# Optimization experiments

Hardware: AMD Instinct MI355X
Metric: run time of the kernel (lower is better)

## Reference

```python
import jax, jax.numpy as jnp
import numpy as np

N = 50000       # nodes
E = 800000      # edges
IN = 64         # input node feature dim
H = 4           # attention heads
C = 32          # per-head channels (h_dim)
HC = H * C      # 128, concat output per conv
ED = 16         # edge feature dim
G = 2000        # number of graphs (molecules)
NEG = 0.2       # GATConv negative slope


def setup_inputs() -> dict:
    key = jax.random.key(0)
    ks = jax.random.split(key, 40)
    rn = lambda k, shp, s=0.1: (jax.random.normal(k, shp, jnp.float32) * s)
    inp = {}
    inp["x"] = jax.random.normal(ks[0], (N, IN), jnp.float32)
    inp["edge_index"] = jax.random.randint(ks[1], (2, E), 0, N)
    inp["edge_attr"] = jax.random.normal(ks[2], (E, ED), jnp.float32)
    inp["batch"] = jnp.sort(jax.random.randint(ks[3], (N,), 0, G))
    dins = [IN, HC, HC]
    i = 4
    for l in (1, 2, 3):
        din = dins[l - 1]
        inp[f"W{l}"] = rn(ks[i], (din, HC)); i += 1
        inp[f"as{l}"] = rn(ks[i], (H, C)); i += 1
        inp[f"ad{l}"] = rn(ks[i], (H, C)); i += 1
        inp[f"We{l}"] = rn(ks[i], (ED, HC)); i += 1
        inp[f"ae{l}"] = rn(ks[i], (H, C)); i += 1
        inp[f"b{l}"] = rn(ks[i], (HC,)); i += 1
    D = 4 * HC
    inp["lw1"] = rn(ks[i], (D, D)); i += 1
    inp["lb1"] = rn(ks[i], (D,)); i += 1
    inp["lw2"] = rn(ks[i], (D, 1)); i += 1
    inp["lb2"] = rn(ks[i], (1,)); i += 1
    return inp


def gat_conv(x, src, dst, edge_attr, W, a_s, a_d, We, a_e, b):
    n = x.shape[0]
    h = (x @ W).reshape(n, H, C)                       # [N,H,C]
    alpha_src = (h * a_s).sum(-1)                      # [N,H]
    alpha_dst = (h * a_d).sum(-1)                      # [N,H]
    he = (edge_attr @ We).reshape(-1, H, C)            # [E,H,C]
    alpha_edge = (he * a_e).sum(-1)                    # [E,H]
    alpha = jax.nn.leaky_relu(alpha_src[src] + alpha_dst[dst] + alpha_edge, NEG)
    # per-destination softmax over incoming edges (stable)
    amax = jax.ops.segment_max(alpha, dst, num_segments=n)
    amax = jnp.where(jnp.isfinite(amax), amax, 0.0)
    ex = jnp.exp(alpha - amax[dst])                    # [E,H]
    denom = jax.ops.segment_sum(ex, dst, num_segments=n)
    w = ex / (denom[dst] + 1e-16)                      # [E,H]
    m = h[src] * w[:, :, None]                         # [E,H,C]
    out = jax.ops.segment_sum(m, dst, num_segments=n)  # [N,H,C]
    return out.reshape(n, HC) + b


def reference(x, edge_index, edge_attr, batch,
              W1, as1, ad1, We1, ae1, b1,
              W2, as2, ad2, We2, ae2, b2,
              W3, as3, ad3, We3, ae3, b3,
              lw1, lb1, lw2, lb2):
    src, dst = edge_index[0], edge_index[1]
    h1 = gat_conv(x, src, dst, edge_attr, W1, as1, ad1, We1, ae1, b1)
    h2 = gat_conv(h1, src, dst, edge_attr, W2, as2, ad2, We2, ae2, b2)
    h3 = gat_conv(h2, src, dst, edge_attr, W3, as3, ad3, We3, ae3, b3)
    h_pool = jax.ops.segment_sum(h3, batch, num_segments=G)  # global_add_pool
    h_pool_ = h_pool[batch]                                  # == repeat_interleave by counts
    h = jnp.concatenate([h1, h2, h3, h_pool_], axis=1)       # [N, 4*HC]
    h = jax.nn.leaky_relu(h @ lw1 + lb1, 0.01)               # torch LeakyReLU default
    return h @ lw2 + lb2                                     # [N, 1]
```

## Files before the change

### kernel.cpp

```cpp
#include <hip/hip_runtime.h>
#include <hip/hip_bf16.h>
#include <math.h>

#define NN 50000
#define NNP 50048
#define NE 800000
#define DIN1 64
#define NHEAD 4
#define CH 32
#define HC 128
#define EDIM 16
#define NG 2000
#define MAXCH 64

typedef __attribute__((ext_vector_type(8))) short short8;
typedef __attribute__((ext_vector_type(4))) float floatx4;

__device__ __forceinline__ float lrelu(float x, float s) { return x > 0.f ? x : s * x; }

__device__ __forceinline__ unsigned short f2bf(float x) {
  unsigned int u = __float_as_uint(x);
  u += 0x7fff + ((u >> 16) & 1);
  return (unsigned short)(u >> 16);
}
__device__ __forceinline__ float bflo(unsigned int u) { return __uint_as_float(u << 16); }
__device__ __forceinline__ float bfhi(unsigned int u) { return __uint_as_float(u & 0xffff0000u); }

__device__ __forceinline__ void async16(void* lds, const void* g) {
  __builtin_amdgcn_global_load_lds((const __attribute__((address_space(1))) unsigned int*)g,
                                   (__attribute__((address_space(3))) unsigned int*)lds, 16, 0, 0);
}

__global__ __launch_bounds__(256) void k_we_a(
    const float* __restrict__ We1, const float* __restrict__ ae1,
    const float* __restrict__ We2, const float* __restrict__ ae2,
    const float* __restrict__ We3, const float* __restrict__ ae3,
    float* __restrict__ we_a) {
  int t = threadIdx.x;
  if (t >= 3 * EDIM * NHEAD) return;
  int l = t / (EDIM * NHEAD);
  int rem = t % (EDIM * NHEAD);
  int d = rem / NHEAD, h = rem % NHEAD;
  const float* We = (l == 0) ? We1 : ((l == 1) ? We2 : We3);
  const float* ae = (l == 0) ? ae1 : ((l == 1) ? ae2 : ae3);
  float s = 0.f;
  for (int c = 0; c < CH; ++c) s += We[d * HC + h * CH + c] * ae[h * CH + c];
  we_a[t] = s;
}

__global__ __launch_bounds__(256) void k_wsd(
    const float* __restrict__ W1, const float* __restrict__ as1, const float* __restrict__ ad1,
    const float* __restrict__ W2, const float* __restrict__ as2, const float* __restrict__ ad2,
    const float* __restrict__ W3, const float* __restrict__ as3, const float* __restrict__ ad3,
    unsigned short* __restrict__ wsdb) {
  int i = blockIdx.x * 256 + threadIdx.x;
  if (i >= 3 * 16 * 128) return;
  int l = i >> 11;
  int col = (i >> 7) & 15;
  int k = i & 127;
  size_t oidx = (size_t)l * 2048 + ((size_t)(k >> 3) * 16 + col) * 8 + (k & 7);
  if (col >= 8 || (l == 0 && k >= DIN1)) { wsdb[oidx] = 0; return; }
  const float* W = (l == 0) ? W1 : ((l == 1) ? W2 : W3);
  int head = col & 3;
  const float* av = (col < 4) ? ((l == 0) ? as1 : ((l == 1) ? as2 : as3))
                              : ((l == 0) ? ad1 : ((l == 1) ? ad2 : ad3));
  float s = 0.f;
  for (int c = 0; c < CH; ++c) s += W[(size_t)k * HC + head * CH + c] * av[head * CH + c];
  wsdb[oidx] = f2bf(s);
}

__global__ __launch_bounds__(256) void k_lw1t(const float* __restrict__ lw1, unsigned short* __restrict__ lw1img) {
  int i = blockIdx.x * 256 + threadIdx.x;
  if (i >= 512 * 384) return;
  int j = i / 384, k = i % 384;
  int jh = j >> 8, jc = j & 255;
  lw1img[((size_t)jh * 48 * 256 + (size_t)(k >> 3) * 256 + jc) * 8 + (k & 7)] = f2bf(lw1[(size_t)k * 512 + j]);
}

__global__ __launch_bounds__(256) void k_wt(const float* __restrict__ W1, const float* __restrict__ W2,
                                            const float* __restrict__ W3, unsigned short* __restrict__ wtb) {
  int i = blockIdx.x * 256 + threadIdx.x;
  if (i >= 128 * 64 + 2 * 128 * 128) return;
  const float* W;
  int j, k;
  size_t base;
  if (i < 128 * 64) {
    W = W1; j = i / 64; k = i % 64; base = 0;
  } else if (i < 128 * 64 + 128 * 128) {
    int ii = i - 128 * 64;
    W = W2; j = ii / 128; k = ii % 128; base = 8192;
  } else {
    int ii = i - (128 * 64 + 128 * 128);
    W = W3; j = ii / 128; k = ii % 128; base = 24576;
  }
  wtb[base + ((size_t)(k >> 3) * 128 + j) * 8 + (k & 7)] = f2bf(W[(size_t)k * HC + j]);
}

__global__ __launch_bounds__(256) void k_cast(const float* __restrict__ x, unsigned short* __restrict__ xb0) {
  int i = blockIdx.x * 256 + threadIdx.x;
  if (i >= NN * DIN1) return;
  int n = i >> 6, k = i & 63;
  xb0[((size_t)(k >> 3) * NNP + n) * 8 + (k & 7)] = f2bf(x[i]);
}

__global__ __launch_bounds__(256) void k_hist(const int* __restrict__ dst, int* __restrict__ cnt) {
  int e = blockIdx.x * 256 + threadIdx.x;
  if (e < NE) atomicAdd(&cnt[dst[e]], 1);
}

__global__ __launch_bounds__(256) void k_scan1(const int* __restrict__ cnt, int* __restrict__ row_start,
                                               int* __restrict__ aux) {
  __shared__ int s[256];
  int t = threadIdx.x;
  int i = blockIdx.x * 256 + t;
  int v = (i < NN) ? cnt[i] : 0;
  s[t] = v;
  __syncthreads();
  for (int off = 1; off < 256; off <<= 1) {
    int tv = (t >= off) ? s[t - off] : 0;
    __syncthreads();
    s[t] += tv;
    __syncthreads();
  }
  if (i < NN) row_start[i] = s[t] - v;
  if (t == 255) aux[blockIdx.x] = s[255];
}

__global__ __launch_bounds__(256) void k_scan2(int* __restrict__ aux, int nb) {
  __shared__ int s[256];
  int t = threadIdx.x;
  int v = (t < nb) ? aux[t] : 0;
  s[t] = v;
  __syncthreads();
  for (int off = 1; off < 256; off <<= 1) {
    int tv = (t >= off) ? s[t - off] : 0;
    __syncthreads();
    s[t] += tv;
    __syncthreads();
  }
  if (t < nb) aux[t] = s[t] - v;
}

__global__ __launch_bounds__(256) void k_scan3(int* __restrict__ row_start, const int* __restrict__ aux) {
  int i = blockIdx.x * 256 + threadIdx.x;
  if (i < NN) row_start[i] += aux[i >> 8];
  else if (i == NN) row_start[NN] = NE;
}

__global__ __launch_bounds__(256) void k_scatter(const int* __restrict__ dst, const int* __restrict__ row_start,
                                                 int* __restrict__ fill, int* __restrict__ perm) {
  int e = blockIdx.x * 256 + threadIdx.x;
  if (e >= NE) return;
  int d = dst[e];
  int p = atomicAdd(&fill[d], 1);
  perm[row_start[d] + p] = e;
}

__global__ __launch_bounds__(256) void k_permute(const int* __restrict__ perm, const int* __restrict__ src,
                                                 const float* __restrict__ edge_attr, const float* __restrict__ wea,
                                                 int* __restrict__ srcp, float* __restrict__ aep) {
  __shared__ float wl[3 * EDIM * NHEAD];
  int t = threadIdx.x;
  if (t < 3 * EDIM * NHEAD) wl[t] = wea[t];
  __syncthreads();
  int pos = blockIdx.x * 256 + t;
  if (pos >= NE) return;
  int e = perm[pos];
  srcp[pos] = src[e];
  float ea[EDIM];
#pragma unroll
  for (int k = 0; k < EDIM; k += 4) {
    float4 v = *(const float4*)&edge_attr[(size_t)e * EDIM + k];
    ea[k] = v.x; ea[k + 1] = v.y; ea[k + 2] = v.z; ea[k + 3] = v.w;
  }
#pragma unroll
  for (int l = 0; l < 3; ++l) {
    float a0 = 0.f, a1 = 0.f, a2 = 0.f, a3 = 0.f;
#pragma unroll
    for (int k = 0; k < EDIM; ++k) {
      float ev = ea[k];
      a0 += ev * wl[l * 64 + k * 4 + 0];
      a1 += ev * wl[l * 64 + k * 4 + 1];
      a2 += ev * wl[l * 64 + k * 4 + 2];
      a3 += ev * wl[l * 64 + k * 4 + 3];
    }
    *(float4*)&aep[(size_t)l * NE * 4 + (size_t)pos * 4] = make_float4(a0, a1, a2, a3);
  }
}

__global__ __launch_bounds__(256) void k_gstart(const int* __restrict__ batch, int* __restrict__ gs) {
  int i = blockIdx.x * 256 + threadIdx.x;
  if (i >= NN) return;
  int b = batch[i];
  if (i == 0) {
    for (int g = 0; g <= b; ++g) gs[g] = 0;
  } else {
    int pb = batch[i - 1];
    for (int g = pb + 1; g <= b; ++g) gs[g] = i;
  }
  if (i == NN - 1) {
    for (int g = b + 1; g <= NG; ++g) gs[g] = NN;
  }
}

template <int K>
__global__ __launch_bounds__(256) void k_conv_mfma(const unsigned short* __restrict__ xin,
                                                   const unsigned short* __restrict__ wt,
                                                   const unsigned short* __restrict__ wsd,
                                                   unsigned short* __restrict__ htb,
                                                   float* __restrict__ asrc, float* __restrict__ adst) {
  __shared__ unsigned short As[512 * 8];
  __shared__ unsigned short Bs[512 * 8];
  __shared__ unsigned short Bs2[64 * 8];
  int t = threadIdx.x;
  int n0 = blockIdx.x * 128;
  int lane = t & 63;
  int wave = t >> 6;
  int wr = wave >> 1, wc = wave & 1;
  int kadd = wave >> 1, rb = (wave & 1) * 64;

  floatx4 acc[4][4];
  floatx4 acce[4];
#pragma unroll
  for (int a = 0; a < 4; ++a) {
    acce[a] = (floatx4){0.f, 0.f, 0.f, 0.f};
#pragma unroll
    for (int b = 0; b < 4; ++b) acc[a][b] = (floatx4){0.f, 0.f, 0.f, 0.f};
  }

  const unsigned short* afp = As + ((size_t)(lane >> 4) * 128 + wr * 64 + (lane & 15)) * 8;
  const unsigned short* bfp = Bs + ((size_t)(lane >> 4) * 128 + wc * 64 + (lane & 15)) * 8;
  const unsigned short* b2fp = Bs2 + ((size_t)(lane >> 4) * 16 + (lane & 15)) * 8;

#pragma unroll
  for (int p = 0; p < 2; ++p) {
    async16(As + (size_t)(p * 256 + wave * 64) * 8,
            xin + ((size_t)(p * 2 + kadd) * NNP + n0 + rb + lane) * 8);
    async16(Bs + (size_t)(p * 256 + wave * 64) * 8,
            wt + ((size_t)(p * 2 + kadd) * 128 + rb + lane) * 8);
  }
  if (wave == 0) async16(Bs2, wsd + (size_t)lane * 8);

  for (int kk = 0; kk < K / 32; ++kk) {
    __syncthreads();
    short8 af[4], bf[4], bf2;
#pragma unroll
    for (int ti = 0; ti < 4; ++ti) af[ti] = *(const short8*)(afp + (size_t)ti * 16 * 8);
#pragma unroll
    for (int tj = 0; tj < 4; ++tj) bf[tj] = *(const short8*)(bfp + (size_t)tj * 16 * 8);
    bf2 = *(const short8*)(b2fp);
    __syncthreads();
    if (kk < K / 32 - 1) {
      int kb = (kk + 1) * 4;
#pragma unroll
      for (int p = 0; p < 2; ++p) {
        async16(As + (size_t)(p * 256 + wave * 64) * 8,
                xin + ((size_t)(kb + p * 2 + kadd) * NNP + n0 + rb + lane) * 8);
        async16(Bs + (size_t)(p * 256 + wave * 64) * 8,
                wt + ((size_t)(kb + p * 2 + kadd) * 128 + rb + lane) * 8);
      }
      if (wave == 0) async16(Bs2, wsd + ((size_t)kb * 16 + lane) * 8);
    }
#pragma unroll
    for (int ti = 0; ti < 4; ++ti)
#pragma unroll
      for (int tj = 0; tj < 4; ++tj)
        acc[ti][tj] = __builtin_amdgcn_mfma_f32_16x16x32_bf16(af[ti], bf[tj], acc[ti][tj], 0, 0, 0);
    if (wc == 0) {
#pragma unroll
      for (int ti = 0; ti < 4; ++ti)
        acce[ti] = __builtin_amdgcn_mfma_f32_16x16x32_bf16(af[ti], bf2, acce[ti], 0, 0, 0);
    }
  }

  int q = lane & 15;
  int colg = wc * 64 + q;
#pragma unroll
  for (int ti = 0; ti < 4; ++ti) {
    int rowb = n0 + wr * 64 + ti * 16 + (lane >> 4) * 4;
#pragma unroll
    for (int r = 0; r < 4; ++r) {
      int row = rowb + r;
      if (row < NN) {
        htb[(size_t)row * HC + colg] = f2bf(acc[ti][0][r]);
        htb[(size_t)row * HC + colg + 16] = f2bf(acc[ti][1][r]);
        htb[(size_t)row * HC + colg + 32] = f2bf(acc[ti][2][r]);
        htb[(size_t)row * HC + colg + 48] = f2bf(acc[ti][3][r]);
        if (wc == 0 && q < 8) {
          float v = acce[ti][r];
          if (q < 4) asrc[row * 4 + q] = v;
          else adst[row * 4 + (q - 4)] = v;
        }
      }
    }
  }
}

__global__ __launch_bounds__(256) void k_aggregate(
    const unsigned short* __restrict__ htb, const int* __restrict__ srcp,
    const float* __restrict__ aep, const float* __restrict__ asrc, const float* __restrict__ adst,
    const int* __restrict__ row_start, const float* __restrict__ bias,
    unsigned short* __restrict__ XBp, int kcoff) {
  __shared__ float exs[4][MAXCH][4];
  __shared__ int cns[4];
  int t = threadIdx.x;
  int lane = t & 63, wid = t >> 6;
  int n = blockIdx.x * 4 + wid;
  bool nok = n < NN;
  int rs = nok ? row_start[n] : 0;
  int re = nok ? row_start[n + 1] : 0;
  int deg = re - rs;
  if (lane == 0) cns[wid] = (deg + MAXCH - 1) / MAXCH;
  __syncthreads();
  int maxc = max(max(cns[0], cns[1]), max(cns[2], cns[3]));
  int q = lane & 15, g = lane >> 4;
  int h = q >> 2;
  float4 ad4 = nok ? *(const float4*)&adst[n * 4] : make_float4(0.f, 0.f, 0.f, 0.f);
  float acc[8];
#pragma unroll
  for (int j = 0; j < 8; ++j) acc[j] = 0.f;
  float d0 = 0.f, d1 = 0.f, d2 = 0.f, d3 = 0.f;

  for (int cc = 0; cc < maxc; ++cc) {
    int base = rs + cc * MAXCH;
    int m = re - base;
    if (m > MAXCH) m = MAXCH;
    if (lane < m) {
      int i = base + lane;
      int s = srcp[i];
      float4 ae = *(const float4*)&aep[(size_t)i * 4];
      float4 as4 = *(const float4*)&asrc[s * 4];
      float4 ex;
      ex.x = __expf(lrelu(as4.x + ad4.x + ae.x, 0.2f));
      ex.y = __expf(lrelu(as4.y + ad4.y + ae.y, 0.2f));
      ex.z = __expf(lrelu(as4.z + ad4.z + ae.z, 0.2f));
      ex.w = __expf(lrelu(as4.w + ad4.w + ae.w, 0.2f));
      *(float4*)&exs[wid][lane][0] = ex;
      d0 += ex.x; d1 += ex.y; d2 += ex.z; d3 += ex.w;
    }
    __syncthreads();
    int iters = (m > 0) ? ((m + 7) >> 3) : 0;
    for (int kk = 0; kk < iters; ++kk) {
      int ii0 = kk * 8 + g;
      int ii1 = ii0 + 4;
      int i0 = base + ((ii0 < m) ? ii0 : 0);
      int i1 = base + ((ii1 < m) ? ii1 : 0);
      int s0 = srcp[i0];
      int s1 = srcp[i1];
      uint4 h0 = *(const uint4*)(htb + (size_t)s0 * HC + q * 8);
      uint4 h1 = *(const uint4*)(htb + (size_t)s1 * HC + q * 8);
      float w0 = (ii0 < m) ? exs[wid][ii0][h] : 0.f;
      float w1 = (ii1 < m) ? exs[wid][ii1][h] : 0.f;
      acc[0] += w0 * bflo(h0.x) + w1 * bflo(h1.x);
      acc[1] += w0 * bfhi(h0.x) + w1 * bfhi(h1.x);
      acc[2] += w0 * bflo(h0.y) + w1 * bflo(h1.y);
      acc[3] += w0 * bfhi(h0.y) + w1 * bfhi(h1.y);
      acc[4] += w0 * bflo(h0.z) + w1 * bflo(h1.z);
      acc[5] += w0 * bfhi(h0.z) + w1 * bfhi(h1.z);
      acc[6] += w0 * bflo(h0.w) + w1 * bflo(h1.w);
      acc[7] += w0 * bfhi(h0.w) + w1 * bfhi(h1.w);
    }
    __syncthreads();
  }

#pragma unroll
  for (int mm = 1; mm < 64; mm <<= 1) {
    d0 += __shfl_xor(d0, mm, 64);
    d1 += __shfl_xor(d1, mm, 64);
    d2 += __shfl_xor(d2, mm, 64);
    d3 += __shfl_xor(d3, mm, 64);
  }
#pragma unroll
  for (int j = 0; j < 8; ++j) {
    acc[j] += __shfl_xor(acc[j], 16, 64);
    acc[j] += __shfl_xor(acc[j], 32, 64);
  }
  if (nok && g == 0) {
    float dh = (h == 0) ? d0 : ((h == 1) ? d1 : ((h == 2) ? d2 : d3));
    float inv = 1.f / (dh + 1e-16f);
    unsigned int w[4];
#pragma unroll
    for (int j = 0; j < 4; ++j) {
      float v0 = acc[2 * j] * inv + bias[q * 8 + 2 * j];
      float v1 = acc[2 * j + 1] * inv + bias[q * 8 + 2 * j + 1];
      w[j] = (unsigned int)f2bf(v0) | ((unsigned int)f2bf(v1) << 16);
    }
    *(uint4*)&XBp[((size_t)(kcoff + q) * NNP + n) * 8] = make_uint4(w[0], w[1], w[2], w[3]);
  }
}

__global__ __launch_bounds__(128) void k_pool(const unsigned short* __restrict__ XBp, const int* __restrict__ gs,
                                              float* __restrict__ hpool) {
  int g = blockIdx.x;
  int j = threadIdx.x;
  int kc = 32 + (j >> 3), sb = j & 7;
  int s = gs[g], e = gs[g + 1];
  float acc = 0.f;
  for (int i = s; i < e; ++i) acc += bflo((unsigned int)XBp[((size_t)kc * NNP + i) * 8 + sb]);
  hpool[(size_t)g * HC + j] = acc;
}

__global__ __launch_bounds__(256) void k_pool_gemm(const float* __restrict__ hpool, const float* __restrict__ lw1,
                                                   float* __restrict__ ph) {
  __shared__ float hp[16][128];
  int t = threadIdx.x;
  int j0 = blockIdx.x * 128;
  int g0 = blockIdx.y * 16;
  int jj = t & 127, gg = t >> 7;
#pragma unroll
  for (int i = 0; i < 8; ++i) {
    int q = t + 256 * i;
    int row = q >> 7, col = q & 127;
    hp[row][col] = hpool[(size_t)(g0 + row) * HC + col];
  }
  __syncthreads();
  float acc[8];
#pragma unroll
  for (int i = 0; i < 8; ++i) acc[i] = 0.f;
  for (int k = 0; k < HC; ++k) {
    float wv = lw1[(size_t)(384 + k) * 512 + j0 + jj];
#pragma unroll
    for (int gi = 0; gi < 8; ++gi) acc[gi] += hp[gg + 2 * gi][k] * wv;
  }
#pragma unroll
  for (int gi = 0; gi < 8; ++gi) ph[(size_t)(g0 + gg + 2 * gi) * 512 + j0 + jj] = acc[gi];
}

__global__ __launch_bounds__(256) void k_outinit(float* __restrict__ out, const float* __restrict__ lb2) {
  int i = blockIdx.x * 256 + threadIdx.x;
  if (i < NN) out[i] = lb2[0];
}

__global__ __launch_bounds__(256, 2) void k_mlp_mfma(
    const unsigned short* __restrict__ XBp, const unsigned short* __restrict__ lw1img,
    const float* __restrict__ ph, const int* __restrict__ batch,
    const float* __restrict__ lb1, const float* __restrict__ lw2,
    float* __restrict__ out) {
  __shared__ unsigned short As[512 * 8];
  __shared__ unsigned short Bs[1024 * 8];
  int t = threadIdx.x;
  int jh = blockIdx.x;
  int n0 = blockIdx.y * 128;
  int lane = t & 63;
  int wave = t >> 6;
  int wr = wave >> 1, wc = wave & 1;
  int kadd = wave >> 1, rb = (wave & 1) * 64;
  const unsigned short* bimg = lw1img + (size_t)jh * 48 * 256 * 8;

  floatx4 acc[4][8];
#pragma unroll
  for (int a = 0; a < 4; ++a)
#pragma unroll
    for (int b = 0; b < 8; ++b) acc[a][b] = (floatx4){0.f, 0.f, 0.f, 0.f};

  const unsigned short* afp = As + ((size_t)(lane >> 4) * 128 + wr * 64 + (lane & 15)) * 8;
  const unsigned short* bfp = Bs + ((size_t)(lane >> 4) * 256 + wc * 128 + (lane & 15)) * 8;

#pragma unroll
  for (int p = 0; p < 2; ++p)
    async16(As + (size_t)(p * 256 + wave * 64) * 8,
            XBp + ((size_t)(p * 2 + kadd) * NNP + n0 + rb + lane) * 8);
#pragma unroll
  for (int p = 0; p < 4; ++p)
    async16(Bs + (size_t)(p * 256 + wave * 64) * 8,
            bimg + ((size_t)p * 256 + wave * 64 + lane) * 8);

  for (int kk = 0; kk < 12; ++kk) {
    __syncthreads();
    short8 af[4], bf[8];
#pragma unroll
    for (int ti = 0; ti < 4; ++ti) af[ti] = *(const short8*)(afp + (size_t)ti * 16 * 8);
#pragma unroll
    for (int tj = 0; tj < 8; ++tj) bf[tj] = *(const short8*)(bfp + (size_t)tj * 16 * 8);
    __syncthreads();
    if (kk < 11) {
      int kb = (kk + 1) * 4;
#pragma unroll
      for (int p = 0; p < 2; ++p)
        async16(As + (size_t)(p * 256 + wave * 64) * 8,
                XBp + ((size_t)(kb + p * 2 + kadd) * NNP + n0 + rb + lane) * 8);
#pragma unroll
      for (int p = 0; p < 4; ++p)
        async16(Bs + (size_t)(p * 256 + wave * 64) * 8,
                bimg + ((size_t)(kb + p) * 256 + wave * 64 + lane) * 8);
    }
#pragma unroll
    for (int ti = 0; ti < 4; ++ti)
#pragma unroll
      for (int tj = 0; tj < 8; ++tj)
        acc[ti][tj] = __builtin_amdgcn_mfma_f32_16x16x32_bf16(af[ti], bf[tj], acc[ti][tj], 0, 0, 0);
  }

  int colg = jh * 256 + wc * 128 + (lane & 15);
#pragma unroll
  for (int ti = 0; ti < 4; ++ti) {
    int rowb = n0 + wr * 64 + ti * 16 + (lane >> 4) * 4;
#pragma unroll
    for (int r = 0; r < 4; ++r) {
      int row = rowb + r;
      int rc = (row < NN) ? row : 0;
      int bg = batch[rc];
      float partial = 0.f;
#pragma unroll
      for (int tj = 0; tj < 8; ++tj) {
        int j = colg + tj * 16;
        float v = acc[ti][tj][r] + ph[(size_t)bg * 512 + j] + lb1[j];
        partial += lrelu(v, 0.01f) * lw2[j];
      }
#pragma unroll
      for (int m = 1; m < 16; m <<= 1) partial += __shfl_xor(partial, m, 16);
      if ((lane & 15) == 0 && row < NN) atomicAdd(&out[row], partial);
    }
  }
}

extern "C" void kernel_launch(void* const* d_in, const int* in_sizes, int n_in,
                              void* d_out, int out_size, void* d_ws, size_t ws_size,
                              hipStream_t stream) {
  const float* x = (const float*)d_in[0];
  const int* edge_index = (const int*)d_in[1];
  const int* src = edge_index;
  const int* dstp = edge_index + NE;
  const float* edge_attr = (const float*)d_in[2];
  const int* batch = (const int*)d_in[3];
  const float* W[3] = {(const float*)d_in[4], (const float*)d_in[10], (const float*)d_in[16]};
  const float* as_[3] = {(const float*)d_in[5], (const float*)d_in[11], (const float*)d_in[17]};
  const float* ad_[3] = {(const float*)d_in[6], (const float*)d_in[12], (const float*)d_in[18]};
  const float* We_[3] = {(const float*)d_in[7], (const float*)d_in[13], (const float*)d_in[19]};
  const float* ae_[3] = {(const float*)d_in[8], (const float*)d_in[14], (const float*)d_in[20]};
  const float* b_[3] = {(const float*)d_in[9], (const float*)d_in[15], (const float*)d_in[21]};
  const float* lw1 = (const float*)d_in[22];
  const float* lb1 = (const float*)d_in[23];
  const float* lw2 = (const float*)d_in[24];
  const float* lb2 = (const float*)d_in[25];
  float* out = (float*)d_out;

  float* f = (float*)d_ws;
  size_t o = 0;
  float* asrc = f + o;  o += (size_t)NN * NHEAD;
  float* adst = f + o;  o += (size_t)NN * NHEAD;
  float* wea = f + o;   o += 256;
  float* hpool = f + o; o += (size_t)NG * HC;
  float* aep = f + o;   o += (size_t)3 * NE * 4;
  unsigned short* xb0 = (unsigned short*)(f + o);
  float* ph = (float*)xb0;
  o += (size_t)8 * NNP * 8 / 2;
  unsigned short* htb = (unsigned short*)(f + o);   o += (size_t)NN * HC / 2;
  unsigned short* XB = (unsigned short*)(f + o);    o += (size_t)48 * NNP * 8 / 2;
  unsigned short* wtb = (unsigned short*)(f + o);   o += (size_t)(128 * 64 + 2 * 128 * 128) / 2;
  unsigned short* lw1img = (unsigned short*)(f + o); o += (size_t)2 * 48 * 256 * 8 / 2;
  unsigned short* wsdb = (unsigned short*)(f + o);  o += (size_t)3 * 2048 / 2;
  int* row_start = (int*)(f + o);
  int* cnt = row_start + (NN + 1);
  int* fill = cnt + NN;
  int* aux = fill + NN;
  int* gs = aux + 256;
  int* perm = gs + (NG + 1);
  int* srcp = perm + NE;

  const int NB = (NN + 255) / 256;
  const int EB = (NE + 255) / 256;

  hipMemsetAsync(cnt, 0, (size_t)2 * NN * sizeof(int), stream);

  k_we_a<<<1, 256, 0, stream>>>(We_[0], ae_[0], We_[1], ae_[1], We_[2], ae_[2], wea);
  k_wsd<<<(3 * 16 * 128 + 255) / 256, 256, 0, stream>>>(W[0], as_[0], ad_[0], W[1], as_[1], ad_[1],
                                                        W[2], as_[2], ad_[2], wsdb);
  k_lw1t<<<(512 * 384 + 255) / 256, 256, 0, stream>>>(lw1, lw1img);
  k_wt<<<(128 * 64 + 2 * 128 * 128 + 255) / 256, 256, 0, stream>>>(W[0], W[1], W[2], wtb);
  k_cast<<<(NN * DIN1 + 255) / 256, 256, 0, stream>>>(x, xb0);
  k_hist<<<EB, 256, 0, stream>>>(dstp, cnt);
  k_scan1<<<NB, 256, 0, stream>>>(cnt, row_start, aux);
  k_scan2<<<1, 256, 0, stream>>>(aux, NB);
  k_scan3<<<NB, 256, 0, stream>>>(row_start, aux);
  k_scatter<<<EB, 256, 0, stream>>>(dstp, row_start, fill, perm);
  k_permute<<<EB, 256, 0, stream>>>(perm, src, edge_attr, wea, srcp, aep);
  k_gstart<<<NB, 256, 0, stream>>>(batch, gs);
  k_outinit<<<NB, 256, 0, stream>>>(out, lb2);

  const int CONVB = NNP / 128;
  unsigned short* wt_l[3] = {wtb, wtb + 8192, wtb + 24576};
  for (int l = 0; l < 3; ++l) {
    unsigned short* wsd_l = wsdb + (size_t)l * 2048;
    const unsigned short* xin = (l == 0) ? xb0 : (XB + (size_t)(l - 1) * 16 * NNP * 8);
    if (l == 0)
      k_conv_mfma<64><<<CONVB, 256, 0, stream>>>(xin, wt_l[0], wsd_l, htb, asrc, adst);
    else
      k_conv_mfma<128><<<CONVB, 256, 0, stream>>>(xin, wt_l[l], wsd_l, htb, asrc, adst);
    k_aggregate<<<(NN + 3) / 4, 256, 0, stream>>>(htb, srcp, aep + (size_t)l * NE * 4, asrc, adst,
                                                  row_start, b_[l], XB, l * 16);
  }

  k_pool<<<NG, 128, 0, stream>>>(XB, gs, hpool);
  k_pool_gemm<<<dim3(4, NG / 16), 256, 0, stream>>>(hpool, lw1, ph);
  k_mlp_mfma<<<dim3(2, NNP / 128), 256, 0, stream>>>(XB, lw1img, ph, batch, lb1, lw2, out);
}
```

Measured before the change: 520.0 us.

## Fuse prep kernels, load full K in conv, double-buffer MLP, drop aggregate block syncs

Merges eight small setup kernels into one block-dispatched prep kernel to cut launch overhead. The conv GEMM now stages the whole K extent into LDS up front with a single barrier, and the MLP GEMM double-buffers its LDS tiles so the next k-chunk loads while the current one computes. The aggregate kernel drops the cross-wave chunk-count sync and uses per-wave loops with block fences instead of barriers, letting each wave exit early. This uses more LDS, and relying on block fences for intra-wave LDS visibility is a correctness risk.

```diff
diff --git a/kernel.cpp b/kernel.cpp
--- a/kernel.cpp
+++ b/kernel.cpp
@@ -31,81 +31,122 @@
                                    (__attribute__((address_space(3))) unsigned int*)lds, 16, 0, 0);
 }
 
-__global__ __launch_bounds__(256) void k_we_a(
+#define NB_WEA 1
+#define NB_WSD 24
+#define NB_LW1T 768
+#define NB_WT 160
+#define NB_CAST 12500
+#define NB_GST 196
+#define NB_OUT 196
+#define NB_HIST 3125
+#define PREP_BLOCKS (NB_WEA + NB_WSD + NB_LW1T + NB_WT + NB_CAST + NB_GST + NB_OUT + NB_HIST)
+
+__global__ __launch_bounds__(256) void k_prep(
     const float* __restrict__ We1, const float* __restrict__ ae1,
     const float* __restrict__ We2, const float* __restrict__ ae2,
-    const float* __restrict__ We3, const float* __restrict__ ae3,
-    float* __restrict__ we_a) {
-  int t = threadIdx.x;
-  if (t >= 3 * EDIM * NHEAD) return;
-  int l = t / (EDIM * NHEAD);
-  int rem = t % (EDIM * NHEAD);
-  int d = rem / NHEAD, h = rem % NHEAD;
-  const float* We = (l == 0) ? We1 : ((l == 1) ? We2 : We3);
-  const float* ae = (l == 0) ? ae1 : ((l == 1) ? ae2 : ae3);
-  float s = 0.f;
-  for (int c = 0; c < CH; ++c) s += We[d * HC + h * CH + c] * ae[h * CH + c];
-  we_a[t] = s;
-}
-
-__global__ __launch_bounds__(256) void k_wsd(
+    const float* __restrict__ We3, const float* __restrict__ ae3, float* __restrict__ wea,
     const float* __restrict__ W1, const float* __restrict__ as1, const float* __restrict__ ad1,
     const float* __restrict__ W2, const float* __restrict__ as2, const float* __restrict__ ad2,
     const float* __restrict__ W3, const float* __restrict__ as3, const float* __restrict__ ad3,
-    unsigned short* __restrict__ wsdb) {
-  int i = blockIdx.x * 256 + threadIdx.x;
-  if (i >= 3 * 16 * 128) return;
-  int l = i >> 11;
-  int col = (i >> 7) & 15;
-  int k = i & 127;
-  size_t oidx = (size_t)l * 2048 + ((size_t)(k >> 3) * 16 + col) * 8 + (k & 7);
-  if (col >= 8 || (l == 0 && k >= DIN1)) { wsdb[oidx] = 0; return; }
-  const float* W = (l == 0) ? W1 : ((l == 1) ? W2 : W3);
-  int head = col & 3;
-  const float* av = (col < 4) ? ((l == 0) ? as1 : ((l == 1) ? as2 : as3))
-                              : ((l == 0) ? ad1 : ((l == 1) ? ad2 : ad3));
-  float s = 0.f;
-  for (int c = 0; c < CH; ++c) s += W[(size_t)k * HC + head * CH + c] * av[head * CH + c];
-  wsdb[oidx] = f2bf(s);
-}
-
-__global__ __launch_bounds__(256) void k_lw1t(const float* __restrict__ lw1, unsigned short* __restrict__ lw1img) {
-  int i = blockIdx.x * 256 + threadIdx.x;
-  if (i >= 512 * 384) return;
-  int j = i / 384, k = i % 384;
-  int jh = j >> 8, jc = j & 255;
-  lw1img[((size_t)jh * 48 * 256 + (size_t)(k >> 3) * 256 + jc) * 8 + (k & 7)] = f2bf(lw1[(size_t)k * 512 + j]);
-}
-
-__global__ __launch_bounds__(256) void k_wt(const float* __restrict__ W1, const float* __restrict__ W2,
-                                            const float* __restrict__ W3, unsigned short* __restrict__ wtb) {
-  int i = blockIdx.x * 256 + threadIdx.x;
-  if (i >= 128 * 64 + 2 * 128 * 128) return;
-  const float* W;
-  int j, k;
-  size_t base;
-  if (i < 128 * 64) {
-    W = W1; j = i / 64; k = i % 64; base = 0;
-  } else if (i < 128 * 64 + 128 * 128) {
-    int ii = i - 128 * 64;
-    W = W2; j = ii / 128; k = ii % 128; base = 8192;
-  } else {
-    int ii = i - (128 * 64 + 128 * 128);
-    W = W3; j = ii / 128; k = ii % 128; base = 24576;
-  }
-  wtb[base + ((size_t)(k >> 3) * 128 + j) * 8 + (k & 7)] = f2bf(W[(size_t)k * HC + j]);
-}
-
-__global__ __launch_bounds__(256) void k_cast(const float* __restrict__ x, unsigned short* __restrict__ xb0) {
-  int i = blockIdx.x * 256 + threadIdx.x;
-  if (i >= NN * DIN1) return;
-  int n = i >> 6, k = i & 63;
-  xb0[((size_t)(k >> 3) * NNP + n) * 8 + (k & 7)] = f2bf(x[i]);
-}
-
-__global__ __launch_bounds__(256) void k_hist(const int* __restrict__ dst, int* __restrict__ cnt) {
-  int e = blockIdx.x * 256 + threadIdx.x;
-  if (e < NE) atomicAdd(&cnt[dst[e]], 1);
+    unsigned short* __restrict__ wsdb,
+    const float* __restrict__ lw1, unsigned short* __restrict__ lw1img,
+    unsigned short* __restrict__ wtb,
+    const float* __restrict__ x, unsigned short* __restrict__ xb0,
+    const int* __restrict__ batch, int* __restrict__ gs,
+    float* __restrict__ out, const float* __restrict__ lb2,
+    const int* __restrict__ dstp, int* __restrict__ cnt) {
+  int b = blockIdx.x;
+  int t = threadIdx.x;
+  if (b < NB_WEA) {
+    if (t >= 3 * EDIM * NHEAD) return;
+    int l = t / (EDIM * NHEAD);
+    int rem = t % (EDIM * NHEAD);
+    int d = rem / NHEAD, h = rem % NHEAD;
+    const float* We = (l == 0) ? We1 : ((l == 1) ? We2 : We3);
+    const float* ae = (l == 0) ? ae1 : ((l == 1) ? ae2 : ae3);
+    float s = 0.f;
+    for (int c = 0; c < CH; ++c) s += We[d * HC + h * CH + c] * ae[h * CH + c];
+    wea[t] = s;
+    return;
+  }
+  b -= NB_WEA;
+  if (b < NB_WSD) {
+    int i = b * 256 + t;
+    int l = i >> 11;
+    int col = (i >> 7) & 15;
+    int k = i & 127;
+    size_t oidx = (size_t)l * 2048 + ((size_t)(k >> 3) * 16 + col) * 8 + (k & 7);
+    if (col >= 8 || (l == 0 && k >= DIN1)) { wsdb[oidx] = 0; return; }
+    const float* W = (l == 0) ? W1 : ((l == 1) ? W2 : W3);
+    int head = col & 3;
+    const float* av = (col < 4) ? ((l == 0) ? as1 : ((l == 1) ? as2 : as3))
+                                : ((l == 0) ? ad1 : ((l == 1) ? ad2 : ad3));
+    float s = 0.f;
+    for (int c = 0; c < CH; ++c) s += W[(size_t)k * HC + head * CH + c] * av[head * CH + c];
+    wsdb[oidx] = f2bf(s);
+    return;
+  }
+  b -= NB_WSD;
+  if (b < NB_LW1T) {
+    int i = b * 256 + t;
+    int j = i / 384, k = i % 384;
+    int jh = j >> 8, jc = j & 255;
+    lw1img[((size_t)jh * 48 * 256 + (size_t)(k >> 3) * 256 + jc) * 8 + (k & 7)] =
+        f2bf(lw1[(size_t)k * 512 + j]);
+    return;
+  }
+  b -= NB_LW1T;
+  if (b < NB_WT) {
+    int i = b * 256 + t;
+    const float* W;
+    int j, k;
+    size_t base;
+    if (i < 128 * 64) {
+      W = W1; j = i / 64; k = i % 64; base = 0;
+    } else if (i < 128 * 64 + 128 * 128) {
+      int ii = i - 128 * 64;
+      W = W2; j = ii / 128; k = ii % 128; base = 8192;
+    } else {
+      int ii = i - (128 * 64 + 128 * 128);
+      W = W3; j = ii / 128; k = ii % 128; base = 24576;
+    }
+    wtb[base + ((size_t)(k >> 3) * 128 + j) * 8 + (k & 7)] = f2bf(W[(size_t)k * HC + j]);
+    return;
+  }
+  b -= NB_WT;
+  if (b < NB_CAST) {
+    int i = b * 256 + t;
+    int n = i >> 6, k = i & 63;
+    xb0[((size_t)(k >> 3) * NNP + n) * 8 + (k & 7)] = f2bf(x[i]);
+    return;
+  }
+  b -= NB_CAST;
+  if (b < NB_GST) {
+    int i = b * 256 + t;
+    if (i >= NN) return;
+    int bb = batch[i];
+    if (i == 0) {
+      for (int g = 0; g <= bb; ++g) gs[g] = 0;
+    } else {
+      int pb = batch[i - 1];
+      for (int g = pb + 1; g <= bb; ++g) gs[g] = i;
+    }
+    if (i == NN - 1) {
+      for (int g = bb + 1; g <= NG; ++g) gs[g] = NN;
+    }
+    return;
+  }
+  b -= NB_GST;
+  if (b < NB_OUT) {
+    int i = b * 256 + t;
+    if (i < NN) out[i] = lb2[0];
+    return;
+  }
+  b -= NB_OUT;
+  {
+    int e = b * 256 + t;
+    if (e < NE) atomicAdd(&cnt[dstp[e]], 1);
+  }
 }
 
 __global__ __launch_bounds__(256) void k_scan1(const int* __restrict__ cnt, int* __restrict__ row_start,
@@ -188,36 +229,23 @@
   }
 }
 
-__global__ __launch_bounds__(256) void k_gstart(const int* __restrict__ batch, int* __restrict__ gs) {
-  int i = blockIdx.x * 256 + threadIdx.x;
-  if (i >= NN) return;
-  int b = batch[i];
-  if (i == 0) {
-    for (int g = 0; g <= b; ++g) gs[g] = 0;
-  } else {
-    int pb = batch[i - 1];
-    for (int g = pb + 1; g <= b; ++g) gs[g] = i;
-  }
-  if (i == NN - 1) {
-    for (int g = b + 1; g <= NG; ++g) gs[g] = NN;
-  }
-}
-
 template <int K>
 __global__ __launch_bounds__(256) void k_conv_mfma(const unsigned short* __restrict__ xin,
                                                    const unsigned short* __restrict__ wt,
                                                    const unsigned short* __restrict__ wsd,
                                                    unsigned short* __restrict__ htb,
                                                    float* __restrict__ asrc, float* __restrict__ adst) {
-  __shared__ unsigned short As[512 * 8];
-  __shared__ unsigned short Bs[512 * 8];
-  __shared__ unsigned short Bs2[64 * 8];
+  constexpr int NC = K / 8;
+  constexpr int CA = NC * 128;
+  constexpr int CB2 = NC * 16;
+  __shared__ unsigned short As[CA * 8];
+  __shared__ unsigned short Bs[CA * 8];
+  __shared__ unsigned short Bs2[CB2 * 8];
   int t = threadIdx.x;
   int n0 = blockIdx.x * 128;
   int lane = t & 63;
   int wave = t >> 6;
   int wr = wave >> 1, wc = wave & 1;
-  int kadd = wave >> 1, rb = (wave & 1) * 64;
 
   floatx4 acc[4][4];
   floatx4 acce[4];
@@ -228,39 +256,26 @@
     for (int b = 0; b < 4; ++b) acc[a][b] = (floatx4){0.f, 0.f, 0.f, 0.f};
   }
 
-  const unsigned short* afp = As + ((size_t)(lane >> 4) * 128 + wr * 64 + (lane & 15)) * 8;
-  const unsigned short* bfp = Bs + ((size_t)(lane >> 4) * 128 + wc * 64 + (lane & 15)) * 8;
-  const unsigned short* b2fp = Bs2 + ((size_t)(lane >> 4) * 16 + (lane & 15)) * 8;
-
-#pragma unroll
-  for (int p = 0; p < 2; ++p) {
-    async16(As + (size_t)(p * 256 + wave * 64) * 8,
-            xin + ((size_t)(p * 2 + kadd) * NNP + n0 + rb + lane) * 8);
-    async16(Bs + (size_t)(p * 256 + wave * 64) * 8,
-            wt + ((size_t)(p * 2 + kadd) * 128 + rb + lane) * 8);
-  }
-  if (wave == 0) async16(Bs2, wsd + (size_t)lane * 8);
-
+  for (int c0 = wave * 64; c0 < CA; c0 += 256) {
+    int kc = c0 >> 7, row0 = c0 & 127;
+    async16(As + (size_t)c0 * 8, xin + ((size_t)kc * NNP + n0 + row0 + lane) * 8);
+    async16(Bs + (size_t)c0 * 8, wt + ((size_t)c0 + lane) * 8);
+  }
+  if (wave * 64 < CB2) async16(Bs2 + (size_t)wave * 64 * 8, wsd + ((size_t)wave * 64 + lane) * 8);
+
+  __syncthreads();
+
+  int frow = lane & 15, fkc = lane >> 4;
+#pragma unroll
   for (int kk = 0; kk < K / 32; ++kk) {
-    __syncthreads();
+    const unsigned short* ab = As + (size_t)(kk * 4 + fkc) * 128 * 8;
+    const unsigned short* bb = Bs + (size_t)(kk * 4 + fkc) * 128 * 8;
     short8 af[4], bf[4], bf2;
 #pragma unroll
-    for (int ti = 0; ti < 4; ++ti) af[ti] = *(const short8*)(afp + (size_t)ti * 16 * 8);
-#pragma unroll
-    for (int tj = 0; tj < 4; ++tj) bf[tj] = *(const short8*)(bfp + (size_t)tj * 16 * 8);
-    bf2 = *(const short8*)(b2fp);
-    __syncthreads();
-    if (kk < K / 32 - 1) {
-      int kb = (kk + 1) * 4;
-#pragma unroll
-      for (int p = 0; p < 2; ++p) {
-        async16(As + (size_t)(p * 256 + wave * 64) * 8,
-                xin + ((size_t)(kb + p * 2 + kadd) * NNP + n0 + rb + lane) * 8);
-        async16(Bs + (size_t)(p * 256 + wave * 64) * 8,
-                wt + ((size_t)(kb + p * 2 + kadd) * 128 + rb + lane) * 8);
-      }
-      if (wave == 0) async16(Bs2, wsd + ((size_t)kb * 16 + lane) * 8);
-    }
+    for (int ti = 0; ti < 4; ++ti) af[ti] = *(const short8*)(ab + ((size_t)(wr * 64 + frow + ti * 16)) * 8);
+#pragma unroll
+    for (int tj = 0; tj < 4; ++tj) bf[tj] = *(const short8*)(bb + ((size_t)(wc * 64 + frow + tj * 16)) * 8);
+    bf2 = *(const short8*)(Bs2 + ((size_t)(kk * 4 + fkc) * 16 + frow) * 8);
 #pragma unroll
     for (int ti = 0; ti < 4; ++ti)
 #pragma unroll
@@ -302,26 +317,21 @@
     const int* __restrict__ row_start, const float* __restrict__ bias,
     unsigned short* __restrict__ XBp, int kcoff) {
   __shared__ float exs[4][MAXCH][4];
-  __shared__ int cns[4];
   int t = threadIdx.x;
   int lane = t & 63, wid = t >> 6;
   int n = blockIdx.x * 4 + wid;
-  bool nok = n < NN;
-  int rs = nok ? row_start[n] : 0;
-  int re = nok ? row_start[n + 1] : 0;
-  int deg = re - rs;
-  if (lane == 0) cns[wid] = (deg + MAXCH - 1) / MAXCH;
-  __syncthreads();
-  int maxc = max(max(cns[0], cns[1]), max(cns[2], cns[3]));
+  if (n >= NN) return;
+  int rs = row_start[n], re = row_start[n + 1];
+  int nchunk = (re - rs + MAXCH - 1) / MAXCH;
   int q = lane & 15, g = lane >> 4;
   int h = q >> 2;
-  float4 ad4 = nok ? *(const float4*)&adst[n * 4] : make_float4(0.f, 0.f, 0.f, 0.f);
+  float4 ad4 = *(const float4*)&adst[n * 4];
   float acc[8];
 #pragma unroll
   for (int j = 0; j < 8; ++j) acc[j] = 0.f;
   float d0 = 0.f, d1 = 0.f, d2 = 0.f, d3 = 0.f;
 
-  for (int cc = 0; cc < maxc; ++cc) {
+  for (int cc = 0; cc < nchunk; ++cc) {
     int base = rs + cc * MAXCH;
     int m = re - base;
     if (m > MAXCH) m = MAXCH;
@@ -338,8 +348,8 @@
       *(float4*)&exs[wid][lane][0] = ex;
       d0 += ex.x; d1 += ex.y; d2 += ex.z; d3 += ex.w;
     }
-    __syncthreads();
-    int iters = (m > 0) ? ((m + 7) >> 3) : 0;
+    __threadfence_block();
+    int iters = (m + 7) >> 3;
     for (int kk = 0; kk < iters; ++kk) {
       int ii0 = kk * 8 + g;
       int ii1 = ii0 + 4;
@@ -360,7 +370,7 @@
       acc[6] += w0 * bflo(h0.w) + w1 * bflo(h1.w);
       acc[7] += w0 * bfhi(h0.w) + w1 * bfhi(h1.w);
     }
-    __syncthreads();
+    __threadfence_block();
   }
 
 #pragma unroll
@@ -375,7 +385,7 @@
     acc[j] += __shfl_xor(acc[j], 16, 64);
     acc[j] += __shfl_xor(acc[j], 32, 64);
   }
-  if (nok && g == 0) {
+  if (g == 0) {
     float dh = (h == 0) ? d0 : ((h == 1) ? d1 : ((h == 2) ? d2 : d3));
     float inv = 1.f / (dh + 1e-16f);
     unsigned int w[4];
@@ -426,18 +436,13 @@
   for (int gi = 0; gi < 8; ++gi) ph[(size_t)(g0 + gg + 2 * gi) * 512 + j0 + jj] = acc[gi];
 }
 
-__global__ __launch_bounds__(256) void k_outinit(float* __restrict__ out, const float* __restrict__ lb2) {
-  int i = blockIdx.x * 256 + threadIdx.x;
-  if (i < NN) out[i] = lb2[0];
-}
-
 __global__ __launch_bounds__(256, 2) void k_mlp_mfma(
     const unsigned short* __restrict__ XBp, const unsigned short* __restrict__ lw1img,
     const float* __restrict__ ph, const int* __restrict__ batch,
     const float* __restrict__ lb1, const float* __restrict__ lw2,
     float* __restrict__ out) {
-  __shared__ unsigned short As[512 * 8];
-  __shared__ unsigned short Bs[1024 * 8];
+  __shared__ unsigned short As[2 * 512 * 8];
+  __shared__ unsigned short Bs[2 * 1024 * 8];
   int t = threadIdx.x;
   int jh = blockIdx.x;
   int n0 = blockIdx.y * 128;
@@ -453,43 +458,39 @@
 #pragma unroll
     for (int b = 0; b < 8; ++b) acc[a][b] = (floatx4){0.f, 0.f, 0.f, 0.f};
 
-  const unsigned short* afp = As + ((size_t)(lane >> 4) * 128 + wr * 64 + (lane & 15)) * 8;
-  const unsigned short* bfp = Bs + ((size_t)(lane >> 4) * 256 + wc * 128 + (lane & 15)) * 8;
-
-#pragma unroll
-  for (int p = 0; p < 2; ++p)
-    async16(As + (size_t)(p * 256 + wave * 64) * 8,
-            XBp + ((size_t)(p * 2 + kadd) * NNP + n0 + rb + lane) * 8);
-#pragma unroll
-  for (int p = 0; p < 4; ++p)
-    async16(Bs + (size_t)(p * 256 + wave * 64) * 8,
-            bimg + ((size_t)p * 256 + wave * 64 + lane) * 8);
-
+#define STAGE(bufv, kbv)                                                                  \
+  do {                                                                                    \
+    const int _bf = (bufv);                                                               \
+    const int _kb = (kbv);                                                                \
+    _Pragma("unroll") for (int pp = 0; pp < 2; ++pp)                                      \
+        async16(As + ((size_t)_bf * 512 + pp * 256 + wave * 64) * 8,                      \
+                XBp + ((size_t)(_kb + pp * 2 + kadd) * NNP + n0 + rb + lane) * 8);        \
+    _Pragma("unroll") for (int pp = 0; pp < 4; ++pp)                                      \
+        async16(Bs + ((size_t)_bf * 1024 + pp * 256 + wave * 64) * 8,                     \
+                bimg + ((size_t)(_kb + pp) * 256 + wave * 64 + lane) * 8);                \
+  } while (0)
+
+  STAGE(0, 0);
+
+  int frow = lane & 15, fkc = lane >> 4;
   for (int kk = 0; kk < 12; ++kk) {
+    int p = kk & 1;
     __syncthreads();
+    const unsigned short* ab = As + (size_t)p * 512 * 8 + ((size_t)fkc * 128 + wr * 64 + frow) * 8;
+    const unsigned short* bb = Bs + (size_t)p * 1024 * 8 + ((size_t)fkc * 256 + wc * 128 + frow) * 8;
     short8 af[4], bf[8];
 #pragma unroll
-    for (int ti = 0; ti < 4; ++ti) af[ti] = *(const short8*)(afp + (size_t)ti * 16 * 8);
-#pragma unroll
-    for (int tj = 0; tj < 8; ++tj) bf[tj] = *(const short8*)(bfp + (size_t)tj * 16 * 8);
-    __syncthreads();
-    if (kk < 11) {
-      int kb = (kk + 1) * 4;
-#pragma unroll
-      for (int p = 0; p < 2; ++p)
-        async16(As + (size_t)(p * 256 + wave * 64) * 8,
-                XBp + ((size_t)(kb + p * 2 + kadd) * NNP + n0 + rb + lane) * 8);
-#pragma unroll
-      for (int p = 0; p < 4; ++p)
-        async16(Bs + (size_t)(p * 256 + wave * 64) * 8,
-                bimg + ((size_t)(kb + p) * 256 + wave * 64 + lane) * 8);
-    }
+    for (int ti = 0; ti < 4; ++ti) af[ti] = *(const short8*)(ab + (size_t)ti * 16 * 8);
+#pragma unroll
+    for (int tj = 0; tj < 8; ++tj) bf[tj] = *(const short8*)(bb + (size_t)tj * 16 * 8);
+    if (kk < 11) STAGE(1 - p, (kk + 1) * 4);
 #pragma unroll
     for (int ti = 0; ti < 4; ++ti)
 #pragma unroll
       for (int tj = 0; tj < 8; ++tj)
         acc[ti][tj] = __builtin_amdgcn_mfma_f32_16x16x32_bf16(af[ti], bf[tj], acc[ti][tj], 0, 0, 0);
   }
+#undef STAGE
 
   int colg = jh * 256 + wc * 128 + (lane & 15);
 #pragma unroll
@@ -563,20 +564,15 @@
 
   hipMemsetAsync(cnt, 0, (size_t)2 * NN * sizeof(int), stream);
 
-  k_we_a<<<1, 256, 0, stream>>>(We_[0], ae_[0], We_[1], ae_[1], We_[2], ae_[2], wea);
-  k_wsd<<<(3 * 16 * 128 + 255) / 256, 256, 0, stream>>>(W[0], as_[0], ad_[0], W[1], as_[1], ad_[1],
-                                                        W[2], as_[2], ad_[2], wsdb);
-  k_lw1t<<<(512 * 384 + 255) / 256, 256, 0, stream>>>(lw1, lw1img);
-  k_wt<<<(128 * 64 + 2 * 128 * 128 + 255) / 256, 256, 0, stream>>>(W[0], W[1], W[2], wtb);
-  k_cast<<<(NN * DIN1 + 255) / 256, 256, 0, stream>>>(x, xb0);
-  k_hist<<<EB, 256, 0, stream>>>(dstp, cnt);
+  k_prep<<<PREP_BLOCKS, 256, 0, stream>>>(
+      We_[0], ae_[0], We_[1], ae_[1], We_[2], ae_[2], wea,
+      W[0], as_[0], ad_[0], W[1], as_[1], ad_[1], W[2], as_[2], ad_[2], wsdb,
+      lw1, lw1img, wtb, x, xb0, batch, gs, out, lb2, dstp, cnt);
   k_scan1<<<NB, 256, 0, stream>>>(cnt, row_start, aux);
   k_scan2<<<1, 256, 0, stream>>>(aux, NB);
   k_scan3<<<NB, 256, 0, stream>>>(row_start, aux);
   k_scatter<<<EB, 256, 0, stream>>>(dstp, row_start, fill, perm);
   k_permute<<<EB, 256, 0, stream>>>(perm, src, edge_attr, wea, srcp, aep);
-  k_gstart<<<NB, 256, 0, stream>>>(batch, gs);
-  k_outinit<<<NB, 256, 0, stream>>>(out, lb2);
 
   const int CONVB = NNP / 128;
   unsigned short* wt_l[3] = {wtb, wtb + 8192, wtb + 24576};
```

Result: faster. 485.7 us (-6.6%).
